# Performance work log

Measured on AMD Instinct MI355X. Metric: run time of the kernel, lower is better.

## Reference

```python
import jax, jax.numpy as jnp
import numpy as np

SIG_G = [1, 1, 1]          # Clifford signature Cl(3,0): 2^3 = 8 blades
N_BLADES = 1 << len(SIG_G)
LAYER_DIMS = [256, 512, 256]
BATCH = 64
ALPHA = 0.1


def _cayley(g):
    """Cayley table C[a,b,k]: e_a * e_b = C[a,b,a^b] * e_{a^b} (blades as bitmasks)."""
    n = len(g)
    K = 1 << n
    C = np.zeros((K, K, K), dtype=np.float32)
    for a in range(K):
        for b in range(K):
            # canonical reordering sign: count generator swaps
            s, aa = 0, a >> 1
            while aa:
                s += bin(aa & b).count('1')
                aa >>= 1
            sign = -1.0 if (s & 1) else 1.0
            # metric contraction for repeated generators
            for i in range(n):
                if (a >> i) & 1 and (b >> i) & 1:
                    sign *= g[i]
            C[a, b, a ^ b] = sign
    return C


def _reverse_signs(n):
    """Reversion sign per blade: (-1)^{r(r-1)/2} for grade r."""
    K = 1 << n
    r = np.array([bin(k).count('1') for k in range(K)])
    return ((-1.0) ** (r * (r - 1) // 2)).astype(np.float32)


CAYLEY = jnp.asarray(_cayley(SIG_G))          # (K, K, K), sparse signed table
REV = jnp.asarray(_reverse_signs(len(SIG_G)))  # (K,)


def geometric_product(A, W, C):
    # A: (B, N, K) multivectors, W: (M, N, K) multivector weights -> (B, M, K)
    # out[b,m,k] = sum_n sum_{a,c} C[a,c,k] * A[b,n,a] * W[m,n,c]
    return jnp.einsum('bna,mnc,ack->bmk', A, W, C)


def setup_inputs() -> dict:
    key = jax.random.key(0)
    k_x, k_w1, k_w2 = jax.random.split(key, 3)
    x = jax.random.normal(k_x, (BATCH, LAYER_DIMS[0], N_BLADES), dtype=jnp.float32)
    w1 = jax.random.normal(k_w1, (LAYER_DIMS[0], LAYER_DIMS[1], N_BLADES), dtype=jnp.float32) * 0.1
    w2 = jax.random.normal(k_w2, (LAYER_DIMS[1], LAYER_DIMS[2], N_BLADES), dtype=jnp.float32) * 0.1
    return {"x": x, "w1": w1, "w2": w2, "n_iter": 20}


def reference(x, w1, w2, n_iter):
    ws = [w1, w2]
    B = x.shape[0]
    # states[0] is detached input (x.detach().clone() in torch)
    states = [jax.lax.stop_gradient(x)]
    for w in ws:
        states.append(jnp.zeros((B, w.shape[1], N_BLADES), dtype=x.dtype))
    for _ in range(n_iter):
        for l in range(1, len(states)):
            w = ws[l - 1]
            x_hat = geometric_product(states[l], w, CAYLEY)          # (B, D_{l-1}, K)
            err = states[l - 1] - x_hat
            w_T = jnp.transpose(w * REV, (1, 0, 2))                  # reverse + transpose
            # torch: grad = -gp(err, w_T); states[l] -= alpha*grad  => += alpha*gp
            states[l] = states[l] + ALPHA * geometric_product(err, w_T, CAYLEY)
    return tuple(states)
```

## Files before the change

### kernel.cpp

```cpp
#include <hip/hip_runtime.h>

typedef unsigned short u16;
typedef __attribute__((ext_vector_type(4))) float f32x4;
typedef __attribute__((ext_vector_type(8))) __bf16 bf16x8;
typedef __attribute__((ext_vector_type(8))) u16 u16x8;

#define ALPHA_F 0.1f

__device__ __host__ constexpr bool SGN(int a, int c) {
  return ((((c & 1) & (((a >> 1) ^ (a >> 2)) & 1)) ^
           (((c >> 1) & 1) & ((a >> 2) & 1))) != 0);
}
__device__ __host__ constexpr float REVF(int c) {
  const int r = (c & 1) + ((c >> 1) & 1) + ((c >> 2) & 1);
  return (r >= 2) ? -1.f : 1.f;
}
__device__ __forceinline__ u16 bf_rnd(float f) {
  unsigned u = __float_as_uint(f);
  return (u16)((u + 0x7FFFu + ((u >> 16) & 1u)) >> 16);
}
__device__ __forceinline__ float bf_val(u16 h) {
  return __uint_as_float(((unsigned)h) << 16);
}
__device__ __forceinline__ f32x4 mf(bf16x8 a, bf16x8 b, f32x4 c) {
  return __builtin_amdgcn_mfma_f32_16x16x32_bf16(a, b, c, 0, 0, 0);
}
__device__ __forceinline__ bf16x8 negf(bf16x8 v) {
  u16x8 u = __builtin_bit_cast(u16x8, v);
  const u16x8 m = {0x8000, 0x8000, 0x8000, 0x8000, 0x8000, 0x8000, 0x8000, 0x8000};
  u = u ^ m;
  return __builtin_bit_cast(bf16x8, u);
}

__global__ __launch_bounds__(256) void pack_in(
    const float* __restrict__ x, const float* __restrict__ w1,
    const float* __restrict__ w2, u16* P1h, u16* P1l, u16* Q1, u16* Qc1,
    u16* P2h, u16* P2l, u16* Q2, u16* Axh, u16* Axl, u16* Vpk2,
    u16* BpAh, u16* BpAl, u16* Z0h, u16* Z0l, float* out0) {
  const int t = blockIdx.x * 256 + threadIdx.x;
  if (t < 131072) {
    const int r = t >> 9, cc = t & 511;
    const float* s = w1 + ((size_t)r * 512 + cc) * 8;
    float v[8];
#pragma unroll
    for (int c = 0; c < 8; ++c) v[c] = s[c];
    const size_t qo = (size_t)((cc >> 4) * 2 + (r >> 7)) * 32768 +
                      ((r >> 5) & 3) * 512 + ((r >> 3) & 3) * 128 +
                      (cc & 15) * 8 + (r & 7);
#pragma unroll
    for (int c = 0; c < 8; ++c) {
      const float q1 = REVF(c) * v[c];
      u16 h = bf_rnd(q1);
      Q1[qo + c * 4096] = h;
      Q1[qo + c * 4096 + 2048] = bf_rnd(q1 - bf_val(h));
      const float qc = ALPHA_F * q1;
      h = bf_rnd(qc);
      Qc1[qo + c * 4096] = h;
      Qc1[qo + c * 4096 + 2048] = bf_rnd(qc - bf_val(h));
    }
  } else if (t < 262144) {
    const int u = t - 131072;
    const int r = u >> 8, c2 = u & 255;
    const float* s = w2 + ((size_t)r * 256 + c2) * 8;
    float v[8];
#pragma unroll
    for (int c = 0; c < 8; ++c) v[c] = s[c];
    const size_t tail = ((r >> 5) & 3) * 512 + ((r >> 3) & 3) * 128 +
                        (c2 & 15) * 8 + (r & 7);
    const size_t qo = (size_t)((c2 >> 4) * 4 + (r >> 7)) * 32768 + tail;
    const size_t wo = (size_t)((c2 >> 4) * 6 + 2 + (r >> 7)) * 32768 + tail;
#pragma unroll
    for (int c = 0; c < 8; ++c) {
      const float q2 = REVF(c) * v[c];
      u16 h = bf_rnd(q2);
      Q2[qo + c * 4096] = h;
      Q2[qo + c * 4096 + 2048] = bf_rnd(q2 - bf_val(h));
      const float qw = ALPHA_F * q2;
      h = bf_rnd(qw);
      const u16 lo = bf_rnd(qw - bf_val(h));
      Vpk2[wo + c * 4096] = h;
      Vpk2[wo + c * 4096 + 2048] = lo;
      const size_t bo = ((size_t)(c * 32 + (c2 >> 3)) * 512 + r) * 8 + (c2 & 7);
      BpAh[bo] = h;
      BpAl[bo] = lo;
    }
  } else if (t < 393216) {
    const int u = t - 262144;
    const int r = u & 255, cc = u >> 8;
    const float* s = w1 + ((size_t)r * 512 + cc) * 8;
#pragma unroll
    for (int a = 0; a < 8; ++a) {
      const float v = s[a];
      const u16 h = bf_rnd(v);
      const size_t o = ((size_t)(a * 32 + (r >> 3)) * 512 + cc) * 8 + (r & 7);
      P1h[o] = h;
      P1l[o] = bf_rnd(v - bf_val(h));
    }
  } else if (t < 524288) {
    const int u = t - 393216;
    const int r = u & 511, c2 = u >> 9;
    const float* s = w2 + ((size_t)r * 256 + c2) * 8;
#pragma unroll
    for (int a = 0; a < 8; ++a) {
      const float v = s[a];
      const u16 h = bf_rnd(v);
      const size_t o = ((size_t)(a * 64 + (r >> 3)) * 256 + c2) * 8 + (r & 7);
      P2h[o] = h;
      P2l[o] = bf_rnd(v - bf_val(h));
    }
  } else if (t < 540672) {
    const int u = t - 524288;
    const int b = u >> 8, n = u & 255;
    const float* s = x + ((size_t)b * 256 + n) * 8;
#pragma unroll
    for (int a = 0; a < 8; ++a) {
      const u16 h = bf_rnd(s[a]);
      const size_t o = ((size_t)(a * 32 + (n >> 3)) * 64 + b) * 8 + (n & 7);
      Axh[o] = h;
      Axl[o] = bf_rnd(s[a] - bf_val(h));
    }
  } else if (t < 573440) {
    const int u = t - 540672;
    ((float4*)out0)[u] = ((const float4*)x)[u];
  } else if (t < 606208) {
    const int u = t - 573440;
    const int hl = u >> 14, i = u & 16383;
    const int a = i >> 11, j = i & 2047;
    const u16x8 z = {0, 0, 0, 0, 0, 0, 0, 0};
    u16* Z = hl ? Z0l : Z0h;
    *(u16x8*)&Z[(size_t)a * 49152 + (size_t)j * 8] = z;
  }
}

__global__ __launch_bounds__(512, 2) void composeK(
    const u16* __restrict__ P1h, const u16* __restrict__ P1l,
    const u16* __restrict__ Q1, const u16* __restrict__ P2h,
    const u16* __restrict__ P2l, const u16* __restrict__ Q2,
    const u16* __restrict__ Axh, const u16* __restrict__ Axl,
    const u16* __restrict__ Qc1, u16* Vpk1, u16* Vpk2,
    u16* V1pAh, u16* V1pAl, u16* UpAh, u16* UpAl,
    u16* Z0h, u16* Z0l, float* c1Z) {
  __shared__ float pan[8][2176];

  const int bid = blockIdx.x, tid = threadIdx.x;
  const int w = tid >> 6, l = tid & 63;
  const int lg = l >> 4, lm = l & 15;

  int seg, rb, p;
  if (bid < 256) { seg = 1; rb = bid & 15; p = bid >> 4; }
  else if (bid < 1280) { seg = 0; rb = (bid - 256) & 31; p = (bid - 256) >> 5; }
  else { seg = 2; rb = (bid - 1280) & 3; p = (bid - 1280) >> 2; }

  const u16* Ah_ = seg == 0 ? P1h : (seg == 1 ? P2h : Axh);
  const u16* Al_ = seg == 0 ? P1l : (seg == 1 ? P2l : Axl);
  const u16* Vb = seg == 0 ? Q1 : (seg == 1 ? Q2 : Qc1);
  const int NROW = seg == 0 ? 512 : (seg == 1 ? 256 : 64);
  const int KC = seg == 1 ? 64 : 32;
  const int NW = seg == 1 ? 2 : 1;
  const int slmul = seg == 1 ? 4 : 2;
  const int row = rb * 16 + lm;

  f32x4 acc[8];
#pragma unroll
  for (int k = 0; k < 8; ++k) acc[k] = f32x4{0.f, 0.f, 0.f, 0.f};

  for (int wi = 0; wi < NW; ++wi) {
    const int n0 = w * (NW * 32) + wi * 32;
    const int sl = n0 >> 7, hst = (n0 >> 5) & 3;
    const u16* Vimg =
        Vb + ((size_t)(p * slmul + sl) << 15) + hst * 512 + lg * 128 + lm * 8;
    const int kc = (n0 >> 3) + lg;
    bf16x8 ah[8], al[8];
#pragma unroll
    for (int a = 0; a < 8; ++a) {
      const size_t o = ((size_t)(a * KC + kc) * NROW + row) * 8;
      ah[a] = *(const bf16x8*)(Ah_ + o);
      al[a] = *(const bf16x8*)(Al_ + o);
    }
    __builtin_amdgcn_s_setprio(1);
#pragma unroll
    for (int c = 0; c < 8; ++c) {
      const bf16x8 vhp = *(const bf16x8*)(Vimg + (size_t)c * 4096);
      const bf16x8 vlp = *(const bf16x8*)(Vimg + (size_t)c * 4096 + 2048);
      const bf16x8 vhn = negf(vhp), vln = negf(vlp);
#pragma unroll
      for (int a = 0; a < 8; ++a) {
        const int k = a ^ c;
        const bf16x8 vh = SGN(a, c) ? vhn : vhp;
        const bf16x8 vl = SGN(a, c) ? vln : vlp;
        acc[k] = mf(ah[a], vh, acc[k]);
        acc[k] = mf(al[a], vh, acc[k]);
        acc[k] = mf(ah[a], vl, acc[k]);
      }
    }
    __builtin_amdgcn_s_setprio(0);
  }

#pragma unroll
  for (int k = 0; k < 8; ++k)
#pragma unroll
    for (int q = 0; q < 4; ++q)
      pan[w][(k * 16 + lg * 4 + q) * 17 + lm] = acc[k][q];
  __syncthreads();

  if (tid < 256) {
    const int k = tid >> 5, rw = (tid >> 1) & 15, ch = tid & 1;
    const int boff = (k * 16 + rw) * 17 + ch * 8;
    f32x4 s0 = {0.f, 0.f, 0.f, 0.f}, s1 = {0.f, 0.f, 0.f, 0.f};
    for (int ss = 0; ss < 8; ++ss) {
      s0 += *(const f32x4*)&pan[ss][boff];
      s1 += *(const f32x4*)&pan[ss][boff + 4];
    }
    float v[8];
#pragma unroll
    for (int e = 0; e < 4; ++e) { v[e] = s0[e]; v[4 + e] = s1[e]; }
    const int n = rb * 16 + rw;

    if (seg <= 1) {
      u16* base = seg == 0 ? Vpk1 : Vpk2;
      const int blk = (seg == 0 ? p * 4 : p * 6) + (n >> 7);
      u16* d = base + ((size_t)blk << 15) + (size_t)k * 4096 +
               ((n >> 5) & 3) * 512 + ((n >> 3) & 3) * 128 + (n & 7);
      u16 ph[8], pl[8];
#pragma unroll
      for (int e = 0; e < 8; ++e) {
        const int m = p * 16 + ch * 8 + e;
        const float val = ((k == 0) && (n == m) ? 1.0f : 0.0f) - ALPHA_F * v[e];
        const u16 hh = bf_rnd(val);
        const u16 ll = bf_rnd(val - bf_val(hh));
        d[(size_t)(ch * 8 + e) * 8] = hh;
        d[2048 + (size_t)(ch * 8 + e) * 8] = ll;
        ph[e] = hh;
        pl[e] = ll;
      }
      if (seg == 0) {
        const size_t po = (((size_t)k * 64 + p * 2 + ch) * 512 + n) * 8;
        *(u16x8*)&V1pAh[po] = *(u16x8*)ph;
        *(u16x8*)&V1pAl[po] = *(u16x8*)pl;
      } else {
        const size_t po = (((size_t)k * 32 + p * 2 + ch) * 256 + n) * 8;
        *(u16x8*)&UpAh[po] = *(u16x8*)ph;
        *(u16x8*)&UpAl[po] = *(u16x8*)pl;
      }
    } else {
      const int b = n;
      float* cp_ = c1Z + (((size_t)k * 64 + p * 2 + ch) * 64 + b) * 8;
      u16x8 h8, l8;
#pragma unroll
      for (int e = 0; e < 8; ++e) {
        cp_[e] = v[e];
        const u16 hh = bf_rnd(v[e]);
        h8[e] = hh;
        l8[e] = bf_rnd(v[e] - bf_val(hh));
      }
      const size_t zo = (((size_t)k * 96 + 32 + p * 2 + ch) * 64 + b) * 8;
      *(u16x8*)&Z0h[zo] = h8;
      *(u16x8*)&Z0l[zo] = l8;
    }
  }
}

struct IArgs {
  const u16 *Zch, *Zcl;
  u16 *Znh, *Znl;
  const u16 *V1, *V2;
  const float *add1, *add2;
  float *oa1, *oa2;
  float *out1, *out2;
  int n_g1;
};

template <bool G1>
__device__ __forceinline__ void iter_body(const IArgs& A, int vbid, int t18,
                                          int fin, float (*pan)[2176]) {
  const int tid = threadIdx.x;
  const int w = tid >> 6, l = tid & 63;
  const int lg = l >> 4, lm = l & 15;
  const int rb = G1 ? vbid : vbid - A.n_g1;
  constexpr int NPAN = G1 ? 32 : 16;
  const int p = rb & (NPAN - 1);
  const int bh = rb / NPAN;
  const int b0 = bh * 16;
  constexpr int KW = G1 ? 64 : 96;
  constexpr int NW = G1 ? 2 : 3;
  constexpr int acb0 = G1 ? 32 : 0;
  constexpr int slmul = G1 ? 4 : 6;
  const u16* Vb = G1 ? A.V1 : A.V2;

  f32x4 acc[8];
#pragma unroll
  for (int k = 0; k < 8; ++k) acc[k] = f32x4{0.f, 0.f, 0.f, 0.f};

#pragma unroll
  for (int wi = 0; wi < NW; ++wi) {
    const int n0 = w * KW + wi * 32;
    const int sl = n0 >> 7, hst = (n0 >> 5) & 3;
    const u16* Vimg = Vb + ((size_t)(p * slmul + sl) << 15) + hst * 512 +
                      lg * 128 + lm * 8;
    const size_t ao = ((size_t)(acb0 + (n0 >> 3) + lg) * 64 + b0 + lm) * 8;
    bf16x8 ah[8], al[8];
#pragma unroll
    for (int a = 0; a < 8; ++a) {
      ah[a] = *(const bf16x8*)(A.Zch + (size_t)a * 49152 + ao);
      al[a] = *(const bf16x8*)(A.Zcl + (size_t)a * 49152 + ao);
    }
    __builtin_amdgcn_s_setprio(1);
#pragma unroll
    for (int c = 0; c < 8; ++c) {
      const bf16x8 vhp = *(const bf16x8*)(Vimg + (size_t)c * 4096);
      const bf16x8 vlp = *(const bf16x8*)(Vimg + (size_t)c * 4096 + 2048);
      const bf16x8 vhn = negf(vhp), vln = negf(vlp);
#pragma unroll
      for (int a = 0; a < 8; ++a) {
        const int k = a ^ c;
        const bf16x8 vh = SGN(a, c) ? vhn : vhp;
        const bf16x8 vl = SGN(a, c) ? vln : vlp;
        acc[k] = mf(ah[a], vh, acc[k]);
        acc[k] = mf(al[a], vh, acc[k]);
        acc[k] = mf(ah[a], vl, acc[k]);
      }
    }
    __builtin_amdgcn_s_setprio(0);
  }

#pragma unroll
  for (int k = 0; k < 8; ++k)
#pragma unroll
    for (int q = 0; q < 4; ++q)
      pan[w][(k * 16 + lg * 4 + q) * 17 + lm] = acc[k][q];
  __syncthreads();

  if (tid < 256) {
    const int k = tid >> 5, row = (tid >> 1) & 15, ch = tid & 1;
    const int boff = (k * 16 + row) * 17 + ch * 8;
    f32x4 s0 = {0.f, 0.f, 0.f, 0.f}, s1 = {0.f, 0.f, 0.f, 0.f};
    for (int ss = 0; ss < 8; ++ss) {
      s0 += *(const f32x4*)&pan[ss][boff];
      s1 += *(const f32x4*)&pan[ss][boff + 4];
    }
    const int b = b0 + row;
    if constexpr (G1) {
      if (A.add1) {
        const float* ca = A.add1 + (((size_t)k * 64 + p * 2 + ch) * 64 + b) * 8;
        s0 += *(const f32x4*)ca;
        s1 += *(const f32x4*)(ca + 4);
      }
    } else {
      if (A.add2) {
        const float* ca = A.add2 + (((size_t)k * 32 + p * 2 + ch) * 64 + b) * 8;
        s0 += *(const f32x4*)ca;
        s1 += *(const f32x4*)(ca + 4);
      }
    }
    float v[8];
#pragma unroll
    for (int e = 0; e < 4; ++e) { v[e] = s0[e]; v[4 + e] = s1[e]; }
    if constexpr (G1) {
      if (A.oa1) {
        float* q = A.oa1 + (((size_t)k * 64 + p * 2 + ch) * 64 + b) * 8;
#pragma unroll
        for (int e = 0; e < 8; ++e) q[e] = v[e];
      }
    } else {
      if (A.oa2) {
        float* q = A.oa2 + (((size_t)k * 32 + p * 2 + ch) * 64 + b) * 8;
#pragma unroll
        for (int e = 0; e < 8; ++e) q[e] = v[e];
      }
    }
    if (!fin) {
      u16x8 h8, l8;
#pragma unroll
      for (int e = 0; e < 8; ++e) {
        const u16 hh = bf_rnd(v[e]);
        h8[e] = hh;
        l8[e] = bf_rnd(v[e] - bf_val(hh));
      }
      const size_t zo =
          (((size_t)k * 96 + (G1 ? 32 : 0) + p * 2 + ch) * 64 + b) * 8;
      *(u16x8*)&A.Znh[zo] = h8;
      *(u16x8*)&A.Znl[zo] = l8;
    }
    if constexpr (G1) {
      if (t18) {
#pragma unroll
        for (int e = 0; e < 8; ++e)
          A.out1[((size_t)b * 512 + p * 16 + ch * 8 + e) * 8 + k] = v[e];
      }
    } else {
      if (fin) {
#pragma unroll
        for (int e = 0; e < 8; ++e)
          A.out2[((size_t)b * 256 + p * 16 + ch * 8 + e) * 8 + k] = v[e];
      }
    }
  }
}

__global__ __launch_bounds__(512, 2) void iter_k(IArgs A, int t18, int fin) {
  __shared__ float pan[8][2176];
  if ((int)blockIdx.x < A.n_g1) iter_body<true>(A, blockIdx.x, t18, fin, pan);
  else iter_body<false>(A, blockIdx.x, t18, fin, pan);
}

struct C2A {
  const u16 *V1pAh, *V1pAl, *UpAh, *UpAl, *BpAh, *BpAl;
  const u16 *Vpk1, *Wcat;
  u16 *V1sqI, *Wcat2;
};

__global__ __launch_bounds__(512) void combo(IArgs S, C2A C) {
  __shared__ float pan[8][2176];
  const int bid = blockIdx.x, tid = threadIdx.x;

  if (bid < 192) {
    if (bid < S.n_g1) iter_body<true>(S, bid, 0, 0, pan);
    else iter_body<false>(S, bid, 0, 0, pan);
    return;
  }
  const int cb = bid - 192;
  const int w = tid >> 6, l = tid & 63;
  const int lg = l >> 4, lm = l & 15;

  if (cb < 512) {
    const int p = cb >> 4, rq = cb & 15;
    const int row0 = rq * 32 + lm, row1 = row0 + 16;
    f32x4 acc0[8], acc1[8];
#pragma unroll
    for (int k = 0; k < 8; ++k) {
      acc0[k] = f32x4{0.f, 0.f, 0.f, 0.f};
      acc1[k] = f32x4{0.f, 0.f, 0.f, 0.f};
    }
#pragma unroll
    for (int wi = 0; wi < 2; ++wi) {
      const int g = w * 2 + wi;
      const u16* Vimg = C.Vpk1 + ((size_t)(p * 4 + (g >> 2)) << 15) +
                        (g & 3) * 512 + lg * 128 + lm * 8;
      const int kc = g * 4 + lg;
      bf16x8 a0h[8], a0l[8], a1h[8], a1l[8];
#pragma unroll
      for (int a = 0; a < 8; ++a) {
        const size_t o0 = ((size_t)(a * 64 + kc) * 512 + row0) * 8;
        const size_t o1 = ((size_t)(a * 64 + kc) * 512 + row1) * 8;
        a0h[a] = *(const bf16x8*)(C.V1pAh + o0);
        a0l[a] = *(const bf16x8*)(C.V1pAl + o0);
        a1h[a] = *(const bf16x8*)(C.V1pAh + o1);
        a1l[a] = *(const bf16x8*)(C.V1pAl + o1);
      }
      __builtin_amdgcn_s_setprio(1);
#pragma unroll
      for (int c = 0; c < 8; ++c) {
        const bf16x8 vhp = *(const bf16x8*)(Vimg + (size_t)c * 4096);
        const bf16x8 vlp = *(const bf16x8*)(Vimg + (size_t)c * 4096 + 2048);
        const bf16x8 vhn = negf(vhp), vln = negf(vlp);
#pragma unroll
        for (int a = 0; a < 8; ++a) {
          const int k = a ^ c;
          const bf16x8 vh = SGN(a, c) ? vhn : vhp;
          const bf16x8 vl = SGN(a, c) ? vln : vlp;
          acc0[k] = mf(a0h[a], vh, acc0[k]);
          acc0[k] = mf(a0l[a], vh, acc0[k]);
          acc0[k] = mf(a0h[a], vl, acc0[k]);
          acc1[k] = mf(a1h[a], vh, acc1[k]);
          acc1[k] = mf(a1l[a], vh, acc1[k]);
          acc1[k] = mf(a1h[a], vl, acc1[k]);
        }
      }
      __builtin_amdgcn_s_setprio(0);
    }
#pragma unroll
    for (int rg = 0; rg < 2; ++rg) {
#pragma unroll
      for (int k = 0; k < 8; ++k)
#pragma unroll
        for (int q = 0; q < 4; ++q)
          pan[w][(k * 16 + lg * 4 + q) * 17 + lm] =
              rg ? acc1[k][q] : acc0[k][q];
      __syncthreads();
      if (tid < 256) {
        const int k = tid >> 5, rw = (tid >> 1) & 15, ch = tid & 1;
        const int boff = (k * 16 + rw) * 17 + ch * 8;
        f32x4 s0 = {0.f, 0.f, 0.f, 0.f}, s1 = {0.f, 0.f, 0.f, 0.f};
        for (int ss = 0; ss < 8; ++ss) {
          s0 += *(const f32x4*)&pan[ss][boff];
          s1 += *(const f32x4*)&pan[ss][boff + 4];
        }
        float v[8];
#pragma unroll
        for (int e = 0; e < 4; ++e) { v[e] = s0[e]; v[4 + e] = s1[e]; }
        const int n = rq * 32 + rg * 16 + rw;
        const int blk = p * 4 + (n >> 7);
        u16* d = C.V1sqI + ((size_t)blk << 15) + (size_t)k * 4096 +
                 ((n >> 5) & 3) * 512 + ((n >> 3) & 3) * 128 + (n & 7);
#pragma unroll
        for (int e = 0; e < 8; ++e) {
          const float val = v[e];
          const u16 hh = bf_rnd(val);
          d[(size_t)(ch * 8 + e) * 8] = hh;
          d[2048 + (size_t)(ch * 8 + e) * 8] = bf_rnd(val - bf_val(hh));
        }
      }
      __syncthreads();
    }
    return;
  }

  int seg, rb, p;
  if (cb < 1024) { seg = 1; rb = (cb - 512) & 31; p = (cb - 512) >> 5; }
  else { seg = 2; rb = (cb - 1024) & 15; p = (cb - 1024) >> 4; }
  const int nwin = seg == 1 ? 3 : 1;
  const int row = rb * 16 + lm;

  f32x4 acc[8];
#pragma unroll
  for (int k = 0; k < 8; ++k) acc[k] = f32x4{0.f, 0.f, 0.f, 0.f};

  for (int wi = 0; wi < nwin; ++wi) {
    const int g = w * nwin + wi;
    const u16 *Aph, *Apl;
    int AKC, AR, kcb;
    const u16* Vimg;
    if (seg == 1) {
      if (g < 8) {
        Aph = C.BpAh; Apl = C.BpAl; AKC = 32; AR = 512; kcb = g * 4;
        Vimg = C.Wcat + ((size_t)(p * 6 + (g >> 2)) << 15) + (g & 3) * 512;
      } else {
        const int g2_ = g - 8;
        Aph = C.V1pAh; Apl = C.V1pAl; AKC = 64; AR = 512; kcb = g2_ * 4;
        Vimg = C.Wcat + ((size_t)(p * 6 + 2 + (g2_ >> 2)) << 15) + (g2_ & 3) * 512;
      }
    } else {
      Aph = C.UpAh; Apl = C.UpAl; AKC = 32; AR = 256; kcb = g * 4;
      Vimg = C.Wcat + ((size_t)(p * 6 + (g >> 2)) << 15) + (g & 3) * 512;
    }
    Vimg += lg * 128 + lm * 8;
    const int kc = kcb + lg;
    bf16x8 ah[8], al[8];
#pragma unroll
    for (int a = 0; a < 8; ++a) {
      const size_t o = ((size_t)(a * AKC + kc) * AR + row) * 8;
      ah[a] = *(const bf16x8*)(Aph + o);
      al[a] = *(const bf16x8*)(Apl + o);
    }
    __builtin_amdgcn_s_setprio(1);
#pragma unroll
    for (int c = 0; c < 8; ++c) {
      const bf16x8 vhp = *(const bf16x8*)(Vimg + (size_t)c * 4096);
      const bf16x8 vlp = *(const bf16x8*)(Vimg + (size_t)c * 4096 + 2048);
      const bf16x8 vhn = negf(vhp), vln = negf(vlp);
#pragma unroll
      for (int a = 0; a < 8; ++a) {
        const int k = a ^ c;
        const bf16x8 vh = SGN(a, c) ? vhn : vhp;
        const bf16x8 vl = SGN(a, c) ? vln : vlp;
        acc[k] = mf(ah[a], vh, acc[k]);
        acc[k] = mf(al[a], vh, acc[k]);
        acc[k] = mf(ah[a], vl, acc[k]);
      }
    }
    __builtin_amdgcn_s_setprio(0);
  }

#pragma unroll
  for (int k = 0; k < 8; ++k)
#pragma unroll
    for (int q = 0; q < 4; ++q)
      pan[w][(k * 16 + lg * 4 + q) * 17 + lm] = acc[k][q];
  __syncthreads();

  if (tid < 256) {
    const int k = tid >> 5, rw = (tid >> 1) & 15, ch = tid & 1;
    const int boff = (k * 16 + rw) * 17 + ch * 8;
    f32x4 s0 = {0.f, 0.f, 0.f, 0.f}, s1 = {0.f, 0.f, 0.f, 0.f};
    for (int ss = 0; ss < 8; ++ss) {
      s0 += *(const f32x4*)&pan[ss][boff];
      s1 += *(const f32x4*)&pan[ss][boff + 4];
    }
    float v[8];
#pragma unroll
    for (int e = 0; e < 4; ++e) { v[e] = s0[e]; v[4 + e] = s1[e]; }
    const int n = rb * 16 + rw;

    const int blk = seg == 1 ? (p * 6 + 2 + (n >> 7)) : (p * 6 + (n >> 7));
    u16* d = C.Wcat2 + ((size_t)blk << 15) + (size_t)k * 4096 +
             ((n >> 5) & 3) * 512 + ((n >> 3) & 3) * 128 + (n & 7);
#pragma unroll
    for (int e = 0; e < 8; ++e) {
      const float val = v[e];
      const u16 hh = bf_rnd(val);
      d[(size_t)(ch * 8 + e) * 8] = hh;
      d[2048 + (size_t)(ch * 8 + e) * 8] = bf_rnd(val - bf_val(hh));
    }
  }
}

extern "C" void kernel_launch(void* const* d_in, const int* in_sizes, int n_in,
                              void* d_out, int out_size, void* d_ws,
                              size_t ws_size, hipStream_t stream) {
  const float* x = (const float*)d_in[0];
  const float* w1 = (const float*)d_in[1];
  const float* w2 = (const float*)d_in[2];

  float* out0 = (float*)d_out;
  float* out1 = out0 + 131072;
  float* out2 = out1 + 262144;

  char* W = (char*)d_ws;
  const size_t MB = 1ull << 20;
  u16* Vpk1 = (u16*)(W);
  u16* Wcat = (u16*)(W + 8 * MB);
  u16* Q1 = (u16*)(W + 14 * MB);
  u16* Q2 = (u16*)(W + 18 * MB);
  u16* Qc1 = (u16*)(W + 22 * MB);
  u16* P1h = (u16*)(W + 26 * MB);
  u16* P1l = (u16*)(W + 28 * MB);
  u16* P2h = (u16*)(W + 30 * MB);
  u16* P2l = (u16*)(W + 32 * MB);
  u16* Axh = (u16*)(W + 34 * MB);
  u16* Axl = (u16*)(W + 34 * MB + 262144);
  float* c1Z = (float*)(W + 35 * MB);
  u16* V1sqI = (u16*)(W + 36 * MB);
  u16* Wcat2 = (u16*)(W + 44 * MB);
  u16* V1pAh = (u16*)(W + 50 * MB);
  u16* V1pAl = (u16*)(W + 54 * MB);
  u16* UpAh = (u16*)(W + 58 * MB);
  u16* UpAl = (u16*)(W + 59 * MB);
  u16* BpAh = (u16*)(W + 60 * MB);
  u16* BpAl = (u16*)(W + 62 * MB);
  float* c1bZ = (float*)(W + 64 * MB);
  float* d2Z = (float*)(W + 65 * MB);
  u16* Z0h = (u16*)(W + 66 * MB);
  u16* Z0l = Z0h + 393216;
  u16* Z1h = Z0h + 786432;
  u16* Z1l = Z0h + 1179648;

  pack_in<<<2368, 256, 0, stream>>>(x, w1, w2, P1h, P1l, Q1, Qc1, P2h, P2l, Q2,
                                    Axh, Axl, Wcat, BpAh, BpAl, Z0h, Z0l, out0);

  composeK<<<1408, 512, 0, stream>>>(P1h, P1l, Q1, P2h, P2l, Q2, Axh, Axl, Qc1,
                                     Vpk1, Wcat, V1pAh, V1pAl, UpAh, UpAl,
                                     Z0h, Z0l, c1Z);

  {
    IArgs seed{Z0h, Z0l, Z1h, Z1l, Vpk1, Wcat, c1Z, nullptr,
               c1bZ, d2Z, out1, out2, 128};
    C2A c2{V1pAh, V1pAl, UpAh, UpAl, BpAh, BpAl, Vpk1, Wcat, V1sqI, Wcat2};
    combo<<<1472, 512, 0, stream>>>(seed, c2);
  }

  for (int tau = 0; tau < 9; ++tau) {
    const bool odd = tau & 1;
    IArgs ia{odd ? Z0h : Z1h, odd ? Z0l : Z1l,
             odd ? Z1h : Z0h, odd ? Z1l : Z0l,
             V1sqI, Wcat2, c1bZ, d2Z, nullptr, nullptr, out1, out2, 128};
    iter_k<<<192, 512, 0, stream>>>(ia, tau == 8 ? 1 : 0, 0);
  }

  {
    IArgs ia{Z0h, Z0l, Z1h, Z1l, Vpk1, Wcat, nullptr, nullptr,
             nullptr, nullptr, out1, out2, 0};
    iter_k<<<64, 512, 0, stream>>>(ia, 0, 1);
  }
}
```

Baseline: 354.6 us.

## Vectorize pack stores and double row tile per block in compose kernel

The packing kernel is remapped so each thread gathers eight rows for one blade and writes contiguous 16-byte vectors, replacing scattered 2-byte stores. The compose kernel now has each block handle 32 rows with two accumulator sets, so every loaded V fragment feeds twice as many MFMAs. This halves the block count for the weight segments and drops the two-blocks-per-CU launch bound. The cost is higher register pressure and lower occupancy, plus serialized two-pass LDS reductions.

```diff
diff --git a/kernel.cpp b/kernel.cpp
--- a/kernel.cpp
+++ b/kernel.cpp
@@ -39,86 +39,115 @@
     u16* BpAh, u16* BpAl, u16* Z0h, u16* Z0l, float* out0) {
   const int t = blockIdx.x * 256 + threadIdx.x;
   if (t < 131072) {
-    const int r = t >> 9, cc = t & 511;
-    const float* s = w1 + ((size_t)r * 512 + cc) * 8;
-    float v[8];
-#pragma unroll
-    for (int c = 0; c < 8; ++c) v[c] = s[c];
-    const size_t qo = (size_t)((cc >> 4) * 2 + (r >> 7)) * 32768 +
-                      ((r >> 5) & 3) * 512 + ((r >> 3) & 3) * 128 +
-                      (cc & 15) * 8 + (r & 7);
-#pragma unroll
-    for (int c = 0; c < 8; ++c) {
-      const float q1 = REVF(c) * v[c];
-      u16 h = bf_rnd(q1);
-      Q1[qo + c * 4096] = h;
-      Q1[qo + c * 4096 + 2048] = bf_rnd(q1 - bf_val(h));
+    const int cc = t & 511;
+    const int ro = (t >> 9) & 31;
+    const int c = t >> 14;
+    u16 h1[8], l1[8], hc[8], lc[8];
+#pragma unroll
+    for (int e = 0; e < 8; ++e) {
+      const int r = ro * 8 + e;
+      const float v = w1[((size_t)r * 512 + cc) * 8 + c];
+      const float q1 = REVF(c) * v;
+      const u16 hh = bf_rnd(q1);
+      h1[e] = hh;
+      l1[e] = bf_rnd(q1 - bf_val(hh));
       const float qc = ALPHA_F * q1;
-      h = bf_rnd(qc);
-      Qc1[qo + c * 4096] = h;
-      Qc1[qo + c * 4096 + 2048] = bf_rnd(qc - bf_val(h));
-    }
+      const u16 hh2 = bf_rnd(qc);
+      hc[e] = hh2;
+      lc[e] = bf_rnd(qc - bf_val(hh2));
+    }
+    const size_t qrun = (size_t)((cc >> 4) * 2 + (ro >> 4)) * 32768 +
+                        ((ro >> 2) & 3) * 512 + (ro & 3) * 128 +
+                        (cc & 15) * 8 + (size_t)c * 4096;
+    *(u16x8*)&Q1[qrun] = *(u16x8*)h1;
+    *(u16x8*)&Q1[qrun + 2048] = *(u16x8*)l1;
+    *(u16x8*)&Qc1[qrun] = *(u16x8*)hc;
+    *(u16x8*)&Qc1[qrun + 2048] = *(u16x8*)lc;
   } else if (t < 262144) {
     const int u = t - 131072;
-    const int r = u >> 8, c2 = u & 255;
-    const float* s = w2 + ((size_t)r * 256 + c2) * 8;
-    float v[8];
-#pragma unroll
-    for (int c = 0; c < 8; ++c) v[c] = s[c];
-    const size_t tail = ((r >> 5) & 3) * 512 + ((r >> 3) & 3) * 128 +
-                        (c2 & 15) * 8 + (r & 7);
-    const size_t qo = (size_t)((c2 >> 4) * 4 + (r >> 7)) * 32768 + tail;
-    const size_t wo = (size_t)((c2 >> 4) * 6 + 2 + (r >> 7)) * 32768 + tail;
-#pragma unroll
-    for (int c = 0; c < 8; ++c) {
-      const float q2 = REVF(c) * v[c];
-      u16 h = bf_rnd(q2);
-      Q2[qo + c * 4096] = h;
-      Q2[qo + c * 4096 + 2048] = bf_rnd(q2 - bf_val(h));
+    const int c2 = u & 255;
+    const int ro = (u >> 8) & 63;
+    const int c = u >> 14;
+    u16 h2[8], l2[8], hw[8], lw[8];
+#pragma unroll
+    for (int e = 0; e < 8; ++e) {
+      const int r = ro * 8 + e;
+      const float v = w2[((size_t)r * 256 + c2) * 8 + c];
+      const float q2 = REVF(c) * v;
+      const u16 hh = bf_rnd(q2);
+      h2[e] = hh;
+      l2[e] = bf_rnd(q2 - bf_val(hh));
       const float qw = ALPHA_F * q2;
-      h = bf_rnd(qw);
-      const u16 lo = bf_rnd(qw - bf_val(h));
-      Vpk2[wo + c * 4096] = h;
-      Vpk2[wo + c * 4096 + 2048] = lo;
+      const u16 hh2 = bf_rnd(qw);
+      hw[e] = hh2;
+      lw[e] = bf_rnd(qw - bf_val(hh2));
+    }
+    const size_t tail = ((ro >> 2) & 3) * 512 + (ro & 3) * 128 +
+                        (c2 & 15) * 8 + (size_t)c * 4096;
+    const size_t qo = (size_t)((c2 >> 4) * 4 + (ro >> 4)) * 32768 + tail;
+    const size_t wo = (size_t)((c2 >> 4) * 6 + 2 + (ro >> 4)) * 32768 + tail;
+    *(u16x8*)&Q2[qo] = *(u16x8*)h2;
+    *(u16x8*)&Q2[qo + 2048] = *(u16x8*)l2;
+    *(u16x8*)&Vpk2[wo] = *(u16x8*)hw;
+    *(u16x8*)&Vpk2[wo + 2048] = *(u16x8*)lw;
+#pragma unroll
+    for (int e = 0; e < 8; ++e) {
+      const int r = ro * 8 + e;
       const size_t bo = ((size_t)(c * 32 + (c2 >> 3)) * 512 + r) * 8 + (c2 & 7);
-      BpAh[bo] = h;
-      BpAl[bo] = lo;
+      BpAh[bo] = hw[e];
+      BpAl[bo] = lw[e];
     }
   } else if (t < 393216) {
     const int u = t - 262144;
-    const int r = u & 255, cc = u >> 8;
-    const float* s = w1 + ((size_t)r * 512 + cc) * 8;
-#pragma unroll
-    for (int a = 0; a < 8; ++a) {
-      const float v = s[a];
+    const int cc = u & 511;
+    const int ro = (u >> 9) & 31;
+    const int a = u >> 14;
+    u16 hh[8], ll[8];
+#pragma unroll
+    for (int e = 0; e < 8; ++e) {
+      const int r = ro * 8 + e;
+      const float v = w1[((size_t)r * 512 + cc) * 8 + a];
       const u16 h = bf_rnd(v);
-      const size_t o = ((size_t)(a * 32 + (r >> 3)) * 512 + cc) * 8 + (r & 7);
-      P1h[o] = h;
-      P1l[o] = bf_rnd(v - bf_val(h));
-    }
+      hh[e] = h;
+      ll[e] = bf_rnd(v - bf_val(h));
+    }
+    const size_t o = ((size_t)(a * 32 + ro) * 512 + cc) * 8;
+    *(u16x8*)&P1h[o] = *(u16x8*)hh;
+    *(u16x8*)&P1l[o] = *(u16x8*)ll;
   } else if (t < 524288) {
     const int u = t - 393216;
-    const int r = u & 511, c2 = u >> 9;
-    const float* s = w2 + ((size_t)r * 256 + c2) * 8;
-#pragma unroll
-    for (int a = 0; a < 8; ++a) {
-      const float v = s[a];
+    const int c2 = u & 255;
+    const int ro = (u >> 8) & 63;
+    const int a = u >> 14;
+    u16 hh[8], ll[8];
+#pragma unroll
+    for (int e = 0; e < 8; ++e) {
+      const int r = ro * 8 + e;
+      const float v = w2[((size_t)r * 256 + c2) * 8 + a];
       const u16 h = bf_rnd(v);
-      const size_t o = ((size_t)(a * 64 + (r >> 3)) * 256 + c2) * 8 + (r & 7);
-      P2h[o] = h;
-      P2l[o] = bf_rnd(v - bf_val(h));
-    }
+      hh[e] = h;
+      ll[e] = bf_rnd(v - bf_val(h));
+    }
+    const size_t o = ((size_t)(a * 64 + ro) * 256 + c2) * 8;
+    *(u16x8*)&P2h[o] = *(u16x8*)hh;
+    *(u16x8*)&P2l[o] = *(u16x8*)ll;
   } else if (t < 540672) {
     const int u = t - 524288;
-    const int b = u >> 8, n = u & 255;
-    const float* s = x + ((size_t)b * 256 + n) * 8;
-#pragma unroll
-    for (int a = 0; a < 8; ++a) {
-      const u16 h = bf_rnd(s[a]);
-      const size_t o = ((size_t)(a * 32 + (n >> 3)) * 64 + b) * 8 + (n & 7);
-      Axh[o] = h;
-      Axl[o] = bf_rnd(s[a] - bf_val(h));
-    }
+    const int b = u & 63;
+    const int no = (u >> 6) & 31;
+    const int a = u >> 11;
+    u16 hh[8], ll[8];
+#pragma unroll
+    for (int e = 0; e < 8; ++e) {
+      const int n = no * 8 + e;
+      const float v = x[((size_t)b * 256 + n) * 8 + a];
+      const u16 h = bf_rnd(v);
+      hh[e] = h;
+      ll[e] = bf_rnd(v - bf_val(h));
+    }
+    const size_t o = ((size_t)(a * 32 + no) * 64 + b) * 8;
+    *(u16x8*)&Axh[o] = *(u16x8*)hh;
+    *(u16x8*)&Axl[o] = *(u16x8*)ll;
   } else if (t < 573440) {
     const int u = t - 540672;
     ((float4*)out0)[u] = ((const float4*)x)[u];
@@ -132,7 +161,7 @@
   }
 }
 
-__global__ __launch_bounds__(512, 2) void composeK(
+__global__ __launch_bounds__(512) void composeK(
     const u16* __restrict__ P1h, const u16* __restrict__ P1l,
     const u16* __restrict__ Q1, const u16* __restrict__ P2h,
     const u16* __restrict__ P2l, const u16* __restrict__ Q2,
@@ -146,36 +175,136 @@
   const int w = tid >> 6, l = tid & 63;
   const int lg = l >> 4, lm = l & 15;
 
-  int seg, rb, p;
-  if (bid < 256) { seg = 1; rb = bid & 15; p = bid >> 4; }
-  else if (bid < 1280) { seg = 0; rb = (bid - 256) & 31; p = (bid - 256) >> 5; }
-  else { seg = 2; rb = (bid - 1280) & 3; p = (bid - 1280) >> 2; }
-
-  const u16* Ah_ = seg == 0 ? P1h : (seg == 1 ? P2h : Axh);
-  const u16* Al_ = seg == 0 ? P1l : (seg == 1 ? P2l : Axl);
-  const u16* Vb = seg == 0 ? Q1 : (seg == 1 ? Q2 : Qc1);
-  const int NROW = seg == 0 ? 512 : (seg == 1 ? 256 : 64);
-  const int KC = seg == 1 ? 64 : 32;
-  const int NW = seg == 1 ? 2 : 1;
-  const int slmul = seg == 1 ? 4 : 2;
-  const int row = rb * 16 + lm;
-
-  f32x4 acc[8];
-#pragma unroll
-  for (int k = 0; k < 8; ++k) acc[k] = f32x4{0.f, 0.f, 0.f, 0.f};
-
-  for (int wi = 0; wi < NW; ++wi) {
-    const int n0 = w * (NW * 32) + wi * 32;
+  if (bid < 640) {
+    const bool isU = bid < 128;
+    const int p = isU ? (bid >> 3) : ((bid - 128) >> 4);
+    const int rq = isU ? (bid & 7) : ((bid - 128) & 15);
+    const int row0 = rq * 32 + lm, row1 = row0 + 16;
+    const int NWf = isU ? 2 : 1;
+    const int slmul = isU ? 4 : 2;
+    const int KCf = isU ? 64 : 32;
+    const int NROWf = isU ? 256 : 512;
+    const u16* Vb = isU ? Q2 : Q1;
+    const u16* Aph = isU ? P2h : P1h;
+    const u16* Apl = isU ? P2l : P1l;
+
+    f32x4 acc0[8], acc1[8];
+#pragma unroll
+    for (int k = 0; k < 8; ++k) {
+      acc0[k] = f32x4{0.f, 0.f, 0.f, 0.f};
+      acc1[k] = f32x4{0.f, 0.f, 0.f, 0.f};
+    }
+    for (int wi = 0; wi < NWf; ++wi) {
+      const int n0 = w * (NWf * 32) + wi * 32;
+      const int sl = n0 >> 7, hst = (n0 >> 5) & 3;
+      const u16* Vimg = Vb + ((size_t)(p * slmul + sl) << 15) + hst * 512 +
+                        lg * 128 + lm * 8;
+      const int kc = (n0 >> 3) + lg;
+      bf16x8 a0h[8], a0l[8], a1h[8], a1l[8];
+#pragma unroll
+      for (int a = 0; a < 8; ++a) {
+        const size_t o0 = ((size_t)(a * KCf + kc) * NROWf + row0) * 8;
+        const size_t o1 = ((size_t)(a * KCf + kc) * NROWf + row1) * 8;
+        a0h[a] = *(const bf16x8*)(Aph + o0);
+        a0l[a] = *(const bf16x8*)(Apl + o0);
+        a1h[a] = *(const bf16x8*)(Aph + o1);
+        a1l[a] = *(const bf16x8*)(Apl + o1);
+      }
+      __builtin_amdgcn_s_setprio(1);
+#pragma unroll
+      for (int c = 0; c < 8; ++c) {
+        const bf16x8 vhp = *(const bf16x8*)(Vimg + (size_t)c * 4096);
+        const bf16x8 vlp = *(const bf16x8*)(Vimg + (size_t)c * 4096 + 2048);
+        const bf16x8 vhn = negf(vhp), vln = negf(vlp);
+#pragma unroll
+        for (int a = 0; a < 8; ++a) {
+          const int k = a ^ c;
+          const bf16x8 vh = SGN(a, c) ? vhn : vhp;
+          const bf16x8 vl = SGN(a, c) ? vln : vlp;
+          acc0[k] = mf(a0h[a], vh, acc0[k]);
+          acc0[k] = mf(a0l[a], vh, acc0[k]);
+          acc0[k] = mf(a0h[a], vl, acc0[k]);
+          acc1[k] = mf(a1h[a], vh, acc1[k]);
+          acc1[k] = mf(a1l[a], vh, acc1[k]);
+          acc1[k] = mf(a1h[a], vl, acc1[k]);
+        }
+      }
+      __builtin_amdgcn_s_setprio(0);
+    }
+#pragma unroll
+    for (int rg = 0; rg < 2; ++rg) {
+#pragma unroll
+      for (int k = 0; k < 8; ++k)
+#pragma unroll
+        for (int q = 0; q < 4; ++q)
+          pan[w][(k * 16 + lg * 4 + q) * 17 + lm] =
+              rg ? acc1[k][q] : acc0[k][q];
+      __syncthreads();
+      if (tid < 256) {
+        const int k = tid >> 5, rw = (tid >> 1) & 15, ch = tid & 1;
+        const int boff = (k * 16 + rw) * 17 + ch * 8;
+        f32x4 s0 = {0.f, 0.f, 0.f, 0.f}, s1 = {0.f, 0.f, 0.f, 0.f};
+        for (int ss = 0; ss < 8; ++ss) {
+          s0 += *(const f32x4*)&pan[ss][boff];
+          s1 += *(const f32x4*)&pan[ss][boff + 4];
+        }
+        float v[8];
+#pragma unroll
+        for (int e = 0; e < 4; ++e) { v[e] = s0[e]; v[4 + e] = s1[e]; }
+        const int n = rq * 32 + rg * 16 + rw;
+
+        u16* base = isU ? Vpk2 : Vpk1;
+        const int blk = (isU ? p * 6 : p * 4) + (n >> 7);
+        u16* d = base + ((size_t)blk << 15) + (size_t)k * 4096 +
+                 ((n >> 5) & 3) * 512 + ((n >> 3) & 3) * 128 + (n & 7);
+        u16 ph[8], pl[8];
+#pragma unroll
+        for (int e = 0; e < 8; ++e) {
+          const int m = p * 16 + ch * 8 + e;
+          const float val =
+              ((k == 0) && (n == m) ? 1.0f : 0.0f) - ALPHA_F * v[e];
+          const u16 hh = bf_rnd(val);
+          const u16 ll = bf_rnd(val - bf_val(hh));
+          d[(size_t)(ch * 8 + e) * 8] = hh;
+          d[2048 + (size_t)(ch * 8 + e) * 8] = ll;
+          ph[e] = hh;
+          pl[e] = ll;
+        }
+        if (isU) {
+          const size_t po = (((size_t)k * 32 + p * 2 + ch) * 256 + n) * 8;
+          *(u16x8*)&UpAh[po] = *(u16x8*)ph;
+          *(u16x8*)&UpAl[po] = *(u16x8*)pl;
+        } else {
+          const size_t po = (((size_t)k * 64 + p * 2 + ch) * 512 + n) * 8;
+          *(u16x8*)&V1pAh[po] = *(u16x8*)ph;
+          *(u16x8*)&V1pAl[po] = *(u16x8*)pl;
+        }
+      }
+      __syncthreads();
+    }
+    return;
+  }
+
+  {
+    const int idx = bid - 640;
+    const int rb = idx & 3, p = idx >> 2;
+    const int row = rb * 16 + lm;
+
+    f32x4 acc[8];
+#pragma unroll
+    for (int k = 0; k < 8; ++k) acc[k] = f32x4{0.f, 0.f, 0.f, 0.f};
+
+    const int n0 = w * 32;
     const int sl = n0 >> 7, hst = (n0 >> 5) & 3;
-    const u16* Vimg =
-        Vb + ((size_t)(p * slmul + sl) << 15) + hst * 512 + lg * 128 + lm * 8;
+    const u16* Vimg = Qc1 + ((size_t)(p * 2 + sl) << 15) + hst * 512 +
+                      lg * 128 + lm * 8;
     const int kc = (n0 >> 3) + lg;
     bf16x8 ah[8], al[8];
 #pragma unroll
     for (int a = 0; a < 8; ++a) {
-      const size_t o = ((size_t)(a * KC + kc) * NROW + row) * 8;
-      ah[a] = *(const bf16x8*)(Ah_ + o);
-      al[a] = *(const bf16x8*)(Al_ + o);
+      const size_t o = ((size_t)(a * 32 + kc) * 64 + row) * 8;
+      ah[a] = *(const bf16x8*)(Axh + o);
+      al[a] = *(const bf16x8*)(Axl + o);
     }
     __builtin_amdgcn_s_setprio(1);
 #pragma unroll
@@ -194,56 +323,26 @@
       }
     }
     __builtin_amdgcn_s_setprio(0);
-  }
-
-#pragma unroll
-  for (int k = 0; k < 8; ++k)
-#pragma unroll
-    for (int q = 0; q < 4; ++q)
-      pan[w][(k * 16 + lg * 4 + q) * 17 + lm] = acc[k][q];
-  __syncthreads();
-
-  if (tid < 256) {
-    const int k = tid >> 5, rw = (tid >> 1) & 15, ch = tid & 1;
-    const int boff = (k * 16 + rw) * 17 + ch * 8;
-    f32x4 s0 = {0.f, 0.f, 0.f, 0.f}, s1 = {0.f, 0.f, 0.f, 0.f};
-    for (int ss = 0; ss < 8; ++ss) {
-      s0 += *(const f32x4*)&pan[ss][boff];
-      s1 += *(const f32x4*)&pan[ss][boff + 4];
-    }
-    float v[8];
-#pragma unroll
-    for (int e = 0; e < 4; ++e) { v[e] = s0[e]; v[4 + e] = s1[e]; }
-    const int n = rb * 16 + rw;
-
-    if (seg <= 1) {
-      u16* base = seg == 0 ? Vpk1 : Vpk2;
-      const int blk = (seg == 0 ? p * 4 : p * 6) + (n >> 7);
-      u16* d = base + ((size_t)blk << 15) + (size_t)k * 4096 +
-               ((n >> 5) & 3) * 512 + ((n >> 3) & 3) * 128 + (n & 7);
-      u16 ph[8], pl[8];
-#pragma unroll
-      for (int e = 0; e < 8; ++e) {
-        const int m = p * 16 + ch * 8 + e;
-        const float val = ((k == 0) && (n == m) ? 1.0f : 0.0f) - ALPHA_F * v[e];
-        const u16 hh = bf_rnd(val);
-        const u16 ll = bf_rnd(val - bf_val(hh));
-        d[(size_t)(ch * 8 + e) * 8] = hh;
-        d[2048 + (size_t)(ch * 8 + e) * 8] = ll;
-        ph[e] = hh;
-        pl[e] = ll;
-      }
-      if (seg == 0) {
-        const size_t po = (((size_t)k * 64 + p * 2 + ch) * 512 + n) * 8;
-        *(u16x8*)&V1pAh[po] = *(u16x8*)ph;
-        *(u16x8*)&V1pAl[po] = *(u16x8*)pl;
-      } else {
-        const size_t po = (((size_t)k * 32 + p * 2 + ch) * 256 + n) * 8;
-        *(u16x8*)&UpAh[po] = *(u16x8*)ph;
-        *(u16x8*)&UpAl[po] = *(u16x8*)pl;
-      }
-    } else {
-      const int b = n;
+
+#pragma unroll
+    for (int k = 0; k < 8; ++k)
+#pragma unroll
+      for (int q = 0; q < 4; ++q)
+        pan[w][(k * 16 + lg * 4 + q) * 17 + lm] = acc[k][q];
+    __syncthreads();
+
+    if (tid < 256) {
+      const int k = tid >> 5, rw = (tid >> 1) & 15, ch = tid & 1;
+      const int boff = (k * 16 + rw) * 17 + ch * 8;
+      f32x4 s0 = {0.f, 0.f, 0.f, 0.f}, s1 = {0.f, 0.f, 0.f, 0.f};
+      for (int ss = 0; ss < 8; ++ss) {
+        s0 += *(const f32x4*)&pan[ss][boff];
+        s1 += *(const f32x4*)&pan[ss][boff + 4];
+      }
+      float v[8];
+#pragma unroll
+      for (int e = 0; e < 4; ++e) { v[e] = s0[e]; v[4 + e] = s1[e]; }
+      const int b = rb * 16 + rw;
       float* cp_ = c1Z + (((size_t)k * 64 + p * 2 + ch) * 64 + b) * 8;
       u16x8 h8, l8;
 #pragma unroll
@@ -637,9 +736,9 @@
   pack_in<<<2368, 256, 0, stream>>>(x, w1, w2, P1h, P1l, Q1, Qc1, P2h, P2l, Q2,
                                     Axh, Axl, Wcat, BpAh, BpAl, Z0h, Z0l, out0);
 
-  composeK<<<1408, 512, 0, stream>>>(P1h, P1l, Q1, P2h, P2l, Q2, Axh, Axl, Qc1,
-                                     Vpk1, Wcat, V1pAh, V1pAl, UpAh, UpAl,
-                                     Z0h, Z0l, c1Z);
+  composeK<<<768, 512, 0, stream>>>(P1h, P1l, Q1, P2h, P2l, Q2, Axh, Axl, Qc1,
+                                    Vpk1, Wcat, V1pAh, V1pAl, UpAh, UpAl,
+                                    Z0h, Z0l, c1Z);
 
   {
     IArgs seed{Z0h, Z0l, Z1h, Z1l, Vpk1, Wcat, c1Z, nullptr,
```

Result: faster. 322.7 us (-9.0%).
